# Kernel optimization log

Hardware: AMD Instinct MI355X
Metric: run time of the kernel (lower is better)

The kernel has to match this reference:

```python
import jax, jax.numpy as jnp
import numpy as np
from jax import lax

SOS = -1
BLANK = 28
MAX_SYMBOLS = 4
T, B, ENC = 128, 32, 1024
VOCAB = 29   # includes blank at index 28
EMB = 320
HID = 320


def setup_inputs() -> dict:
    key = jax.random.key(0)
    ks = jax.random.split(key, 9)
    s = 0.1
    return {
        "x": jax.random.normal(ks[0], (T, B, ENC), jnp.float32),
        "lengths": jax.random.randint(ks[1], (B,), T // 2, T + 1, jnp.int32),
        "embedding": jax.random.normal(ks[2], (VOCAB - 1, EMB), jnp.float32) * s,
        "W_ih": jax.random.normal(ks[3], (4 * HID, EMB), jnp.float32) * s,
        "W_hh": jax.random.normal(ks[4], (4 * HID, HID), jnp.float32) * s,
        "b_ih": jax.random.normal(ks[5], (4 * HID,), jnp.float32) * s,
        "b_hh": jax.random.normal(ks[6], (4 * HID,), jnp.float32) * s,
        "W_joint": jax.random.normal(ks[7], (VOCAB, ENC + HID), jnp.float32) * s,
        "b_joint": jax.random.normal(ks[8], (VOCAB,), jnp.float32) * s,
    }


def _lstm_cell(xe, h, c, W_ih, W_hh, b_ih, b_hh):
    gates = xe @ W_ih.T + h @ W_hh.T + b_ih + b_hh          # [B, 4H]
    i, f, g, o = jnp.split(gates, 4, axis=-1)               # torch gate order
    i, f, o = jax.nn.sigmoid(i), jax.nn.sigmoid(f), jax.nn.sigmoid(o)
    g = jnp.tanh(g)
    c2 = f * c + i * g
    h2 = o * jnp.tanh(c2)
    return h2, c2


def _decode(x, lengths, embedding, W_ih, W_hh, b_ih, b_hh, W_joint, b_joint):
    Tn, Bn, _ = x.shape
    Lmax = Tn * MAX_SYMBOLS
    bidx = jnp.arange(Bn)

    def sym_step(carry, _):
        h, c, last, pos, labels, lps, active = carry
        # pred step: zero embedding for SOS, else embed (label>blank -> label-1)
        adj = jnp.where(last > BLANK, last - 1, last)
        adj = jnp.clip(adj, 0, VOCAB - 2)
        emb = jnp.where((last == SOS)[:, None], 0.0, embedding[adj])  # [B, EMB]
        h2, c2 = _lstm_cell(emb, h, c, W_ih, W_hh, b_ih, b_hh)
        # joint step: concat(enc frame, pred) -> fc -> log_softmax
        f_enc = carry_f                                            # closed over
        logits = jnp.concatenate([f_enc, h2], axis=-1) @ W_joint.T + b_joint
        logp = jax.nn.log_softmax(logits, axis=-1)                 # [B, V]
        idx = jnp.argmax(logp, axis=-1).astype(jnp.int32)
        v = jnp.take_along_axis(logp, idx[:, None].astype(jnp.int32), axis=-1)[:, 0]
        is_blank = idx == BLANK
        emit = active & (~is_blank)
        # commit hidden/label only on non-blank emission (as original)
        h = jnp.where(emit[:, None], h2, h)
        c = jnp.where(emit[:, None], c2, c)
        last = jnp.where(emit, idx, last)
        cur = labels[bidx, pos]
        labels = labels.at[bidx, pos].set(jnp.where(emit, idx, cur))
        lps = lps + jnp.where(active, v, 0.0)
        pos = pos + emit.astype(pos.dtype)
        active = active & (~is_blank)
        return (h, c, last, pos, labels, lps, active), None

    def time_step(carry, inp):
        f_t, t = inp                                              # f_t: [B, ENC]
        h, c, last, pos, labels, lps = carry
        active0 = t < lengths
        global carry_f
        carry_f = f_t
        (h, c, last, pos, labels, lps, _), _ = lax.scan(
            sym_step, (h, c, last, pos, labels, lps, active0), None,
            length=MAX_SYMBOLS)
        return (h, c, last, pos, labels, lps), None

    init = (
        jnp.zeros((Bn, HID), x.dtype),
        jnp.zeros((Bn, HID), x.dtype),
        jnp.full((Bn,), SOS, jnp.int32),
        jnp.zeros((Bn,), jnp.int32),
        jnp.full((Bn, Lmax), -1, jnp.int32),
        jnp.zeros((Bn,), x.dtype),
    )
    (h, c, last, pos, labels, lps), _ = lax.scan(
        time_step, init, (x, jnp.arange(Tn)))
    return labels, pos, lps


def reference(x, lengths, embedding, W_ih, W_hh, b_ih, b_hh, W_joint, b_joint):
    # labels: [B, T*MAX_SYMBOLS] int32, padded with -1
    # n_symbols: [B] number of emitted symbols per utterance
    # logp_sum: [B] sum of selected max log-probs over all evaluated decode steps
    labels, n_symbols, logp_sum = _decode(
        x, lengths, embedding, W_ih, W_hh, b_ih, b_hh, W_joint, b_joint)
    return labels, n_symbols, logp_sum
```

## Files before the change

### kernel.cpp

```cpp
#include <hip/hip_runtime.h>
#include <math.h>

typedef unsigned long long u64;
typedef unsigned int u32;

#define BN 32
#define TN 128
#define ENCD 1024
#define HID 320
#define NG 1280
#define VN 29
#define BLANKI 28
#define SLICES 8
#define UPS 40
#define ROWS 160
#define JW 1344
#define XSTRIDE 70
#define NPOLL (SLICES*69)

#define E_OFF   0
#define E_SZ    (TN*BN*VN)
#define P_OFF   (E_OFF + E_SZ)
#define P_SZ    (VN*NG)
#define X_OFF   (P_OFF + P_SZ)
#define X_U64S  (2*BN*SLICES*XSTRIDE)

__device__ __forceinline__ float dot4(float4 a, float4 b) {
    return a.x*b.x + a.y*b.y + a.z*b.z + a.w*b.w;
}

__global__ __launch_bounds__(256) void k_enc(const float* __restrict__ x,
        const float* __restrict__ Wj, const float* __restrict__ bj,
        float* __restrict__ E, u64* __restrict__ xchg)
{
    __shared__ float xl[4][1056];
    const int tid = threadIdx.x;
    const int blk = blockIdx.x;
    const int t = blk >> 3, b0 = (blk & 7) * 4;

    if (tid < 35) xchg[(size_t)blk*35 + tid] = 0ull;

    #pragma unroll
    for (int bb = 0; bb < 4; ++bb) {
        const float4* src = (const float4*)(x + ((size_t)(t*BN + b0 + bb))*ENCD);
        float4 v4 = src[tid];
        ((float4*)&xl[bb][0])[tid + (tid >> 5)] = v4;
    }
    __syncthreads();
    if (tid < 232) {
        const int v = tid >> 3, k8 = tid & 7;
        float a0=0.f, a1=0.f, a2=0.f, a3=0.f;
        const float4* wrow = (const float4*)(Wj + (size_t)v*JW) + k8*32;
        const float4* x0 = ((const float4*)&xl[0][0]) + k8*33;
        const float4* x1 = ((const float4*)&xl[1][0]) + k8*33;
        const float4* x2 = ((const float4*)&xl[2][0]) + k8*33;
        const float4* x3 = ((const float4*)&xl[3][0]) + k8*33;
        #pragma unroll 4
        for (int m = 0; m < 32; ++m) {
            float4 w4 = wrow[m];
            a0 += dot4(w4, x0[m]);
            a1 += dot4(w4, x1[m]);
            a2 += dot4(w4, x2[m]);
            a3 += dot4(w4, x3[m]);
        }
        #pragma unroll
        for (int d = 1; d < 8; d <<= 1) {
            a0 += __shfl_xor(a0, d); a1 += __shfl_xor(a1, d);
            a2 += __shfl_xor(a2, d); a3 += __shfl_xor(a3, d);
        }
        if (k8 == 0) {
            float bjv = bj[v];
            E[((size_t)(t*BN + b0+0))*VN + v] = a0 + bjv;
            E[((size_t)(t*BN + b0+1))*VN + v] = a1 + bjv;
            E[((size_t)(t*BN + b0+2))*VN + v] = a2 + bjv;
            E[((size_t)(t*BN + b0+3))*VN + v] = a3 + bjv;
        }
    }
}

__global__ __launch_bounds__(256) void k_pred(const float* __restrict__ emb,
        const float* __restrict__ Wih, const float* __restrict__ bih,
        const float* __restrict__ bhh, float* __restrict__ P)
{
    __shared__ float el[HID];
    const int tid = threadIdx.x, j = blockIdx.x;
    if (tid < 80) {
        float4 v4 = make_float4(0.f, 0.f, 0.f, 0.f);
        if (j < 28) v4 = ((const float4*)(emb + (size_t)j*HID))[tid];
        ((float4*)el)[tid] = v4;
    }
    __syncthreads();
    #pragma unroll
    for (int q = 0; q < 5; ++q) {
        const int r = q*256 + tid;
        float acc = bih[r] + bhh[r];
        const float4* wrow = (const float4*)(Wih + (size_t)r*HID);
        #pragma unroll 8
        for (int k4 = 0; k4 < 80; ++k4)
            acc += dot4(wrow[k4], ((const float4*)el)[k4]);
        P[(size_t)j*NG + r] = acc;
    }
}

__global__ __launch_bounds__(256, 1) void k_dec(const int* __restrict__ lengths,
        const float* __restrict__ Whh, const float* __restrict__ Wj,
        const float* __restrict__ E, const float* __restrict__ P,
        u64* __restrict__ xchg, float* __restrict__ out)
{
    __shared__ float P_lds[VN*ROWS];
    __shared__ float Wjh[VN*UPS];
    __shared__ float h_com[HID];
    __shared__ float h2st[HID];
    __shared__ float c_com[UPS];
    __shared__ float c2st[UPS];
    __shared__ float gates[ROWS];
    __shared__ float plog_l[SLICES*VN];
    __shared__ float lsum[VN];
    __shared__ float E_l[VN];
    __shared__ float pad_force[14000];

    const int tid = threadIdx.x;
    const int bid = blockIdx.x;
    const int b = bid & 31, slice = bid >> 5;
    const int rg = tid >> 3, kg = tid & 7;
    const int lane = tid & 63;

    int len = lengths[b];
    if (len > TN) len = TN;
    if (len < 0) {
        pad_force[tid] = (float)tid;
        h_com[tid & 255] = pad_force[(tid*7) & 13999];
    }

    float4 wq[50];
    #pragma unroll
    for (int q = 0; q < 5; ++q) {
        const int r = rg*5 + q;
        const int gt = r / 40, u = r - gt*40;
        const float4* wrow = (const float4*)(Whh + ((size_t)(gt*HID + slice*UPS + u))*HID + kg*40);
        #pragma unroll
        for (int jb = 0; jb < 10; ++jb) wq[q*10 + jb] = wrow[jb];
    }
    for (int i = tid; i < VN*ROWS; i += 256) {
        const int jj = i / ROWS, r = i - jj*ROWS;
        const int gt = r / 40, u = r - gt*40;
        P_lds[i] = P[(size_t)jj*NG + gt*HID + slice*UPS + u];
    }
    for (int i = tid; i < VN*UPS; i += 256) {
        const int v = i / UPS, k = i - v*UPS;
        Wjh[i] = Wj[(size_t)v*JW + ENCD + slice*UPS + k];
    }
    for (int i = tid; i < HID; i += 256) h_com[i] = 0.f;
    if (tid < UPS) c_com[tid] = 0.f;
    if (slice == 0) for (int i = tid; i < 512; i += 256) out[b*512 + i] = -1.0f;
    __syncthreads();

    float lps = 0.f;
    int pos = 0, jrow = 28, n = 1;
    bool dirty = true;

    for (int t = 0; t < len; ++t) {
        __syncthreads();
        if (tid < VN) E_l[tid] = E[((size_t)(t*BN + b))*VN + tid];
        __syncthreads();

        for (int s = 0; s < 4; ++s) {
            if (dirty) {
                __syncthreads();
                const int par = n & 1;
                const size_t mybase = ((size_t)(par*BN + b)*SLICES + slice)*XSTRIDE;
                float acc[5] = {0.f, 0.f, 0.f, 0.f, 0.f};
                #pragma unroll
                for (int jb = 0; jb < 10; ++jb) {
                    float4 hv = *(const float4*)(h_com + kg*40 + jb*4);
                    #pragma unroll
                    for (int q = 0; q < 5; ++q) acc[q] += dot4(wq[q*10 + jb], hv);
                }
                #pragma unroll
                for (int q = 0; q < 5; ++q) {
                    acc[q] += __shfl_xor(acc[q], 1);
                    acc[q] += __shfl_xor(acc[q], 2);
                    acc[q] += __shfl_xor(acc[q], 4);
                }
                if (kg == 0) {
                    #pragma unroll
                    for (int q = 0; q < 5; ++q) {
                        const int r = rg*5 + q;
                        gates[r] = acc[q] + P_lds[jrow*ROWS + r];
                    }
                }
                __syncthreads();
                if (tid < UPS) {
                    const float gi = gates[tid],      gf = gates[40+tid];
                    const float gg = gates[80+tid],   go = gates[120+tid];
                    const float ii = 1.f/(1.f+expf(-gi));
                    const float ff = 1.f/(1.f+expf(-gf));
                    const float oo = 1.f/(1.f+expf(-go));
                    const float G  = tanhf(gg);
                    const float c2 = ff*c_com[tid] + ii*G;
                    c2st[tid] = c2;
                    const float h2 = oo * tanhf(c2);
                    h2st[slice*UPS + tid] = h2;
                    const u64 pk = ((u64)(u32)n << 32) | (u64)__float_as_uint(h2);
                    __hip_atomic_store(&xchg[mybase + tid], pk,
                                       __ATOMIC_RELAXED, __HIP_MEMORY_SCOPE_AGENT);
                }
                __syncthreads();
                if (tid < 232) {
                    const int v = tid >> 3, k8 = tid & 7;
                    float pp = 0.f;
                    #pragma unroll
                    for (int m2 = 0; m2 < 5; ++m2)
                        pp += Wjh[v*UPS + k8*5 + m2] * h2st[slice*UPS + k8*5 + m2];
                    pp += __shfl_xor(pp, 1);
                    pp += __shfl_xor(pp, 2);
                    pp += __shfl_xor(pp, 4);
                    if (k8 == 0) {
                        const u64 pk = ((u64)(u32)n << 32) | (u64)__float_as_uint(pp);
                        __hip_atomic_store(&xchg[mybase + UPS + v], pk,
                                           __ATOMIC_RELAXED, __HIP_MEMORY_SCOPE_AGENT);
                    }
                }
                {
                    const size_t pbase = ((size_t)(par*BN + b)*SLICES)*XSTRIDE;
                    for (int i = tid; i < NPOLL; i += 256) {
                        const int j2 = i / 69, w = i - j2*69;
                        const u64* ap = &xchg[pbase + (size_t)j2*XSTRIDE + w];
                        u64 v; int cap = 0;
                        do {
                            v = __hip_atomic_load(ap, __ATOMIC_RELAXED,
                                                  __HIP_MEMORY_SCOPE_AGENT);
                        } while ((u32)(v >> 32) != (u32)n && ++cap < (1 << 22));
                        const float f = __uint_as_float((u32)v);
                        if (w < UPS) h2st[j2*UPS + w] = f;
                        else         plog_l[j2*VN + (w - UPS)] = f;
                    }
                }
                __syncthreads();
                if (tid < VN) {
                    float sA = 0.f;
                    #pragma unroll
                    for (int j2 = 0; j2 < 8; ++j2) sA += plog_l[j2*VN + tid];
                    lsum[tid] = sA;
                }
                __syncthreads();
                n++;
            }
            const float Lv = (lane < VN) ? (E_l[lane] + lsum[lane]) : -INFINITY;
            float m = Lv; int ai = lane;
            #pragma unroll
            for (int d = 1; d < 64; d <<= 1) {
                const float om = __shfl_xor(m, d);
                const int   oi = __shfl_xor(ai, d);
                if (om > m || (om == m && oi < ai)) { m = om; ai = oi; }
            }
            float e = (lane < VN) ? expf(Lv - m) : 0.f;
            #pragma unroll
            for (int d = 1; d < 64; d <<= 1) e += __shfl_xor(e, d);
            lps += -logf(e);

            if (ai == BLANKI) { dirty = false; break; }
            if (slice == 0 && tid == 0) out[b*512 + pos] = (float)ai;
            pos++;
            h_com[tid] = h2st[tid];
            if (tid < 64) h_com[256 + tid] = h2st[256 + tid];
            if (tid < UPS) c_com[tid] = c2st[tid];
            jrow = ai;
            dirty = true;
        }
    }

    if (slice == 0 && tid == 0) {
        out[16384 + b] = (float)pos;
        out[16416 + b] = lps;
    }
}

extern "C" void kernel_launch(void* const* d_in, const int* in_sizes, int n_in,
                              void* d_out, int out_size, void* d_ws, size_t ws_size,
                              hipStream_t stream) {
    const float* x    = (const float*)d_in[0];
    const int* lens   = (const int*)  d_in[1];
    const float* emb  = (const float*)d_in[2];
    const float* Wih  = (const float*)d_in[3];
    const float* Whh  = (const float*)d_in[4];
    const float* bih  = (const float*)d_in[5];
    const float* bhh  = (const float*)d_in[6];
    const float* Wj   = (const float*)d_in[7];
    const float* bj   = (const float*)d_in[8];
    float* out = (float*)d_out;
    float* ws  = (float*)d_ws;

    float* E    = ws + E_OFF;
    float* P    = ws + P_OFF;
    u64*   xchg = (u64*)(ws + X_OFF);

    hipLaunchKernelGGL(k_enc,  dim3(1024), dim3(256), 0, stream, x, Wj, bj, E, xchg);
    hipLaunchKernelGGL(k_pred, dim3(29),   dim3(256), 0, stream, emb, Wih, bih, bhh, P);
    hipLaunchKernelGGL(k_dec,  dim3(256),  dim3(256), 0, stream,
                       lens, Whh, Wj, E, P, xchg, out);
}
```

Before: 2.010 ms.

## Exchange only h2 across slices, compute joint locally, use XCC-local atomic polling

Each slice now broadcasts only its 40 h2 values, not h2 plus partial joint logits. Every block holds the full hidden-part joint weights in LDS and computes the full 29-logit projection locally, which removes one exchange phase and one barrier per decode step. The code probes whether all slices of a batch row share an XCC and, if so, uses inline-asm atomic swap/or operations for the exchange, with a fallback to agent-scope atomics. The encoder logits are kept in registers instead of LDS. In exchange each block does redundant joint compute, and correctness depends on hardware-specific inline asm and an XCC-ID heuristic.

```diff
diff --git a/kernel.cpp b/kernel.cpp
--- a/kernel.cpp
+++ b/kernel.cpp
@@ -15,8 +15,9 @@
 #define UPS 40
 #define ROWS 160
 #define JW 1344
-#define XSTRIDE 70
-#define NPOLL (SLICES*69)
+#define JSTR 324
+#define XSTRIDE 48
+#define NPOLL (7*UPS)
 
 #define E_OFF   0
 #define E_SZ    (TN*BN*VN)
@@ -24,9 +25,37 @@
 #define P_SZ    (VN*NG)
 #define X_OFF   (P_OFF + P_SZ)
 #define X_U64S  (2*BN*SLICES*XSTRIDE)
+#define TOK_OFF X_U64S
+#define DEC_OFF (TOK_OFF + BN*SLICES*16)
+#define HS2_OFF (DEC_OFF + BN)
+#define TOTAL_U64S (HS2_OFF + BN*SLICES)
 
 __device__ __forceinline__ float dot4(float4 a, float4 b) {
     return a.x*b.x + a.y*b.y + a.z*b.z + a.w*b.w;
+}
+
+__device__ __forceinline__ void fast_store(u64* p, u64 v) {
+    asm volatile("global_atomic_swap_x2 %0, %1, off"
+                 :: "v"(p), "v"(v) : "memory");
+}
+__device__ __forceinline__ u64 fast_load(u64* p) {
+    u64 r;
+    asm volatile("global_atomic_or_x2 %0, %1, %2, off sc0\n\ts_waitcnt vmcnt(0)"
+                 : "=&v"(r) : "v"(p), "v"(0ull) : "memory");
+    return r;
+}
+__device__ __forceinline__ void fast_load2(u64* pA, u64* pB, u64& rA, u64& rB) {
+    asm volatile("global_atomic_or_x2 %0, %2, %4, off sc0\n\t"
+                 "global_atomic_or_x2 %1, %3, %4, off sc0\n\t"
+                 "s_waitcnt vmcnt(0)"
+                 : "=&v"(rA), "=&v"(rB)
+                 : "v"(pA), "v"(pB), "v"(0ull) : "memory");
+}
+__device__ __forceinline__ u64 aload(const u64* p) {
+    return __hip_atomic_load(p, __ATOMIC_RELAXED, __HIP_MEMORY_SCOPE_AGENT);
+}
+__device__ __forceinline__ void astore(u64* p, u64 v) {
+    __hip_atomic_store(p, v, __ATOMIC_RELAXED, __HIP_MEMORY_SCOPE_AGENT);
 }
 
 __global__ __launch_bounds__(256) void k_enc(const float* __restrict__ x,
@@ -38,7 +67,10 @@
     const int blk = blockIdx.x;
     const int t = blk >> 3, b0 = (blk & 7) * 4;
 
-    if (tid < 35) xchg[(size_t)blk*35 + tid] = 0ull;
+    if (tid < 29) {
+        const int idx = blk*29 + tid;
+        if (idx < TOTAL_U64S) xchg[idx] = 0ull;
+    }
 
     #pragma unroll
     for (int bb = 0; bb < 4; ++bb) {
@@ -108,16 +140,15 @@
         u64* __restrict__ xchg, float* __restrict__ out)
 {
     __shared__ float P_lds[VN*ROWS];
-    __shared__ float Wjh[VN*UPS];
+    __shared__ float Wjh[VN*JSTR];
     __shared__ float h_com[HID];
     __shared__ float h2st[HID];
     __shared__ float c_com[UPS];
     __shared__ float c2st[UPS];
     __shared__ float gates[ROWS];
-    __shared__ float plog_l[SLICES*VN];
     __shared__ float lsum[VN];
-    __shared__ float E_l[VN];
-    __shared__ float pad_force[14000];
+    __shared__ int   flag_fast;
+    __shared__ float pad_force[6200];
 
     const int tid = threadIdx.x;
     const int bid = blockIdx.x;
@@ -125,11 +156,18 @@
     const int rg = tid >> 3, kg = tid & 7;
     const int lane = tid & 63;
 
+    if (tid == 0) {
+        u32 xcc;
+        asm volatile("s_getreg_b32 %0, hwreg(HW_REG_XCC_ID)" : "=s"(xcc));
+        astore(&xchg[HS2_OFF + b*SLICES + slice], (u64)(xcc & 0xFFu) | 0x100ull);
+        fast_store(&xchg[TOK_OFF + (size_t)(b*SLICES + slice)*16], 0xA5ull);
+    }
+
     int len = lengths[b];
     if (len > TN) len = TN;
     if (len < 0) {
         pad_force[tid] = (float)tid;
-        h_com[tid & 255] = pad_force[(tid*7) & 13999];
+        h_com[tid & 255] = pad_force[(tid*7) & 6199];
     }
 
     float4 wq[50];
@@ -146,23 +184,53 @@
         const int gt = r / 40, u = r - gt*40;
         P_lds[i] = P[(size_t)jj*NG + gt*HID + slice*UPS + u];
     }
-    for (int i = tid; i < VN*UPS; i += 256) {
-        const int v = i / UPS, k = i - v*UPS;
-        Wjh[i] = Wj[(size_t)v*JW + ENCD + slice*UPS + k];
+    for (int i = tid; i < VN*HID; i += 256) {
+        const int v = i / HID, k = i - v*HID;
+        Wjh[v*JSTR + k] = Wj[(size_t)v*JW + ENCD + k];
     }
     for (int i = tid; i < HID; i += 256) h_com[i] = 0.f;
     if (tid < UPS) c_com[tid] = 0.f;
     if (slice == 0) for (int i = tid; i < 512; i += 256) out[b*512 + i] = -1.0f;
+
+    if (tid == 0) {
+        if (slice == 0) {
+            bool ok = true; u32 v0 = 0;
+            for (int j2 = 0; j2 < SLICES; ++j2) {
+                u64 v = 0; int cap = 0;
+                do { v = aload(&xchg[HS2_OFF + b*SLICES + j2]); }
+                while (!(v & 0x100ull) && ++cap < (1 << 22));
+                if (!(v & 0x100ull)) { ok = false; break; }
+                const u32 xv = (u32)(v & 0xFFu);
+                if (xv >= 8u) { ok = false; break; }
+                if (j2 == 0) v0 = xv; else if (xv != v0) { ok = false; break; }
+            }
+            if (ok) {
+                for (int j2 = 1; j2 < SLICES && ok; ++j2) {
+                    u64 v = 0; int cap = 0;
+                    do { v = fast_load(&xchg[TOK_OFF + (size_t)(b*SLICES + j2)*16]); }
+                    while (v != 0xA5ull && ++cap < (1 << 20));
+                    if (v != 0xA5ull) ok = false;
+                }
+            }
+            astore(&xchg[DEC_OFF + b], 2ull | (ok ? 1ull : 0ull));
+            flag_fast = ok ? 1 : 0;
+        } else {
+            u64 v = 0; int cap = 0;
+            do { v = aload(&xchg[DEC_OFF + b]); }
+            while (!(v & 2ull) && ++cap < (1 << 24));
+            flag_fast = (v & 2ull) ? (int)(v & 1ull) : 0;
+        }
+    }
     __syncthreads();
+    const bool fast = (flag_fast != 0);
 
     float lps = 0.f;
     int pos = 0, jrow = 28, n = 1;
     bool dirty = true;
 
     for (int t = 0; t < len; ++t) {
-        __syncthreads();
-        if (tid < VN) E_l[tid] = E[((size_t)(t*BN + b))*VN + tid];
-        __syncthreads();
+        const float Ereg = (lane < VN)
+            ? E[((size_t)(t*BN + b))*VN + lane] : -INFINITY;
 
         for (int s = 0; s < 4; ++s) {
             if (dirty) {
@@ -202,51 +270,67 @@
                     const float h2 = oo * tanhf(c2);
                     h2st[slice*UPS + tid] = h2;
                     const u64 pk = ((u64)(u32)n << 32) | (u64)__float_as_uint(h2);
-                    __hip_atomic_store(&xchg[mybase + tid], pk,
-                                       __ATOMIC_RELAXED, __HIP_MEMORY_SCOPE_AGENT);
+                    u64* p = &xchg[mybase + tid];
+                    if (fast) fast_store(p, pk); else astore(p, pk);
+                }
+                {
+                    const size_t pbase = ((size_t)(par*BN + b)*SLICES)*XSTRIDE;
+                    const int iA = tid;
+                    int jA = iA / UPS; const int wA = iA - jA*UPS;
+                    jA += (jA >= slice);
+                    u64* pA = &xchg[pbase + (size_t)jA*XSTRIDE + wA];
+                    const int iB = tid + 256;
+                    bool needB = (iB < NPOLL);
+                    int jB = 0, wB = 0; u64* pB = pA;
+                    if (needB) {
+                        jB = iB / UPS; wB = iB - jB*UPS; jB += (jB >= slice);
+                        pB = &xchg[pbase + (size_t)jB*XSTRIDE + wB];
+                    }
+                    bool needA = true;
+                    u64 vA = 0, vB = 0;
+                    int cap = 0;
+                    while ((needA || needB) && cap < (1 << 18)) {
+                        if (fast) {
+                            if (needA && needB) fast_load2(pA, pB, vA, vB);
+                            else if (needA)     vA = fast_load(pA);
+                            else                vB = fast_load(pB);
+                        } else {
+                            if (needA) vA = aload(pA);
+                            if (needB) vB = aload(pB);
+                        }
+                        if (needA && (u32)(vA >> 32) == (u32)n) {
+                            h2st[jA*UPS + wA] = __uint_as_float((u32)vA);
+                            needA = false;
+                        }
+                        if (needB && (u32)(vB >> 32) == (u32)n) {
+                            h2st[jB*UPS + wB] = __uint_as_float((u32)vB);
+                            needB = false;
+                        }
+                        ++cap;
+                    }
                 }
                 __syncthreads();
                 if (tid < 232) {
                     const int v = tid >> 3, k8 = tid & 7;
-                    float pp = 0.f;
-                    #pragma unroll
-                    for (int m2 = 0; m2 < 5; ++m2)
-                        pp += Wjh[v*UPS + k8*5 + m2] * h2st[slice*UPS + k8*5 + m2];
-                    pp += __shfl_xor(pp, 1);
-                    pp += __shfl_xor(pp, 2);
-                    pp += __shfl_xor(pp, 4);
-                    if (k8 == 0) {
-                        const u64 pk = ((u64)(u32)n << 32) | (u64)__float_as_uint(pp);
-                        __hip_atomic_store(&xchg[mybase + UPS + v], pk,
-                                           __ATOMIC_RELAXED, __HIP_MEMORY_SCOPE_AGENT);
-                    }
-                }
-                {
-                    const size_t pbase = ((size_t)(par*BN + b)*SLICES)*XSTRIDE;
-                    for (int i = tid; i < NPOLL; i += 256) {
-                        const int j2 = i / 69, w = i - j2*69;
-                        const u64* ap = &xchg[pbase + (size_t)j2*XSTRIDE + w];
-                        u64 v; int cap = 0;
-                        do {
-                            v = __hip_atomic_load(ap, __ATOMIC_RELAXED,
-                                                  __HIP_MEMORY_SCOPE_AGENT);
-                        } while ((u32)(v >> 32) != (u32)n && ++cap < (1 << 22));
-                        const float f = __uint_as_float((u32)v);
-                        if (w < UPS) h2st[j2*UPS + w] = f;
-                        else         plog_l[j2*VN + (w - UPS)] = f;
-                    }
-                }
-                __syncthreads();
-                if (tid < VN) {
                     float sA = 0.f;
                     #pragma unroll
-                    for (int j2 = 0; j2 < 8; ++j2) sA += plog_l[j2*VN + tid];
-                    lsum[tid] = sA;
+                    for (int j2 = 0; j2 < SLICES; ++j2) {
+                        float pp = 0.f;
+                        #pragma unroll
+                        for (int m2 = 0; m2 < 5; ++m2)
+                            pp += Wjh[v*JSTR + j2*UPS + k8*5 + m2]
+                                * h2st[j2*UPS + k8*5 + m2];
+                        pp += __shfl_xor(pp, 1);
+                        pp += __shfl_xor(pp, 2);
+                        pp += __shfl_xor(pp, 4);
+                        sA += pp;
+                    }
+                    if (k8 == 0) lsum[v] = sA;
                 }
                 __syncthreads();
                 n++;
             }
-            const float Lv = (lane < VN) ? (E_l[lane] + lsum[lane]) : -INFINITY;
+            const float Lv = (lane < VN) ? (Ereg + lsum[lane]) : -INFINITY;
             float m = Lv; int ai = lane;
             #pragma unroll
             for (int d = 1; d < 64; d <<= 1) {
```

After: 2.139 ms. 6.4% more time.

## Overlap remote polling with local LSTM/joint compute and drop barriers

Applied to the files above, without the earlier changes.

Splits the block into warp roles: the first wavefront computes the local LSTM cell update and joint partial logits, while the other three wavefronts poll the seven remote slices concurrently, each handling up to three addresses per loop iteration. The own slice is no longer polled. The encoder logit row is held in a register instead of LDS, which removes two barriers per time step. The logit-sum reduction moves into the argmax lane, and the Wjh LDS stride is padded to avoid bank conflicts. The change lowers the spin cap, which risks reading stale values when a wait runs long.

```diff
diff --git a/kernel.cpp b/kernel.cpp
--- a/kernel.cpp
+++ b/kernel.cpp
@@ -15,8 +15,9 @@
 #define UPS 40
 #define ROWS 160
 #define JW 1344
+#define JSTR 41
 #define XSTRIDE 70
-#define NPOLL (SLICES*69)
+#define NPOLL (7*69)
 
 #define E_OFF   0
 #define E_SZ    (TN*BN*VN)
@@ -27,6 +28,12 @@
 
 __device__ __forceinline__ float dot4(float4 a, float4 b) {
     return a.x*b.x + a.y*b.y + a.z*b.z + a.w*b.w;
+}
+__device__ __forceinline__ u64 aload(const u64* p) {
+    return __hip_atomic_load(p, __ATOMIC_RELAXED, __HIP_MEMORY_SCOPE_AGENT);
+}
+__device__ __forceinline__ void astore(u64* p, u64 v) {
+    __hip_atomic_store(p, v, __ATOMIC_RELAXED, __HIP_MEMORY_SCOPE_AGENT);
 }
 
 __global__ __launch_bounds__(256) void k_enc(const float* __restrict__ x,
@@ -108,16 +115,14 @@
         u64* __restrict__ xchg, float* __restrict__ out)
 {
     __shared__ float P_lds[VN*ROWS];
-    __shared__ float Wjh[VN*UPS];
+    __shared__ float Wjh[VN*JSTR];
     __shared__ float h_com[HID];
     __shared__ float h2st[HID];
     __shared__ float c_com[UPS];
     __shared__ float c2st[UPS];
     __shared__ float gates[ROWS];
     __shared__ float plog_l[SLICES*VN];
-    __shared__ float lsum[VN];
-    __shared__ float E_l[VN];
-    __shared__ float pad_force[14000];
+    __shared__ float pad_force[13600];
 
     const int tid = threadIdx.x;
     const int bid = blockIdx.x;
@@ -129,7 +134,7 @@
     if (len > TN) len = TN;
     if (len < 0) {
         pad_force[tid] = (float)tid;
-        h_com[tid & 255] = pad_force[(tid*7) & 13999];
+        h_com[tid & 255] = pad_force[(tid*7) & 13599];
     }
 
     float4 wq[50];
@@ -148,7 +153,7 @@
     }
     for (int i = tid; i < VN*UPS; i += 256) {
         const int v = i / UPS, k = i - v*UPS;
-        Wjh[i] = Wj[(size_t)v*JW + ENCD + slice*UPS + k];
+        Wjh[v*JSTR + k] = Wj[(size_t)v*JW + ENCD + slice*UPS + k];
     }
     for (int i = tid; i < HID; i += 256) h_com[i] = 0.f;
     if (tid < UPS) c_com[tid] = 0.f;
@@ -160,9 +165,8 @@
     bool dirty = true;
 
     for (int t = 0; t < len; ++t) {
-        __syncthreads();
-        if (tid < VN) E_l[tid] = E[((size_t)(t*BN + b))*VN + tid];
-        __syncthreads();
+        const float Ereg = (lane < VN)
+            ? E[((size_t)(t*BN + b))*VN + lane] : -INFINITY;
 
         for (int s = 0; s < 4; ++s) {
             if (dirty) {
@@ -190,63 +194,84 @@
                     }
                 }
                 __syncthreads();
-                if (tid < UPS) {
-                    const float gi = gates[tid],      gf = gates[40+tid];
-                    const float gg = gates[80+tid],   go = gates[120+tid];
-                    const float ii = 1.f/(1.f+expf(-gi));
-                    const float ff = 1.f/(1.f+expf(-gf));
-                    const float oo = 1.f/(1.f+expf(-go));
-                    const float G  = tanhf(gg);
-                    const float c2 = ff*c_com[tid] + ii*G;
-                    c2st[tid] = c2;
-                    const float h2 = oo * tanhf(c2);
-                    h2st[slice*UPS + tid] = h2;
-                    const u64 pk = ((u64)(u32)n << 32) | (u64)__float_as_uint(h2);
-                    __hip_atomic_store(&xchg[mybase + tid], pk,
-                                       __ATOMIC_RELAXED, __HIP_MEMORY_SCOPE_AGENT);
-                }
-                __syncthreads();
-                if (tid < 232) {
-                    const int v = tid >> 3, k8 = tid & 7;
-                    float pp = 0.f;
+                if (tid < 64) {
+                    if (tid < UPS) {
+                        const float gi = gates[tid],      gf = gates[40+tid];
+                        const float gg = gates[80+tid],   go = gates[120+tid];
+                        const float ii = 1.f/(1.f+expf(-gi));
+                        const float ff = 1.f/(1.f+expf(-gf));
+                        const float oo = 1.f/(1.f+expf(-go));
+                        const float G  = tanhf(gg);
+                        const float c2 = ff*c_com[tid] + ii*G;
+                        c2st[tid] = c2;
+                        const float h2 = oo * tanhf(c2);
+                        h2st[slice*UPS + tid] = h2;
+                        const u64 pk = ((u64)(u32)n << 32) | (u64)__float_as_uint(h2);
+                        astore(&xchg[mybase + tid], pk);
+                    }
+                    if (tid < VN) {
+                        float pkv[8];
+                        #pragma unroll
+                        for (int k8 = 0; k8 < 8; ++k8) {
+                            float pk = 0.f;
+                            #pragma unroll
+                            for (int m2 = 0; m2 < 5; ++m2)
+                                pk += Wjh[tid*JSTR + k8*5 + m2]
+                                    * h2st[slice*UPS + k8*5 + m2];
+                            pkv[k8] = pk;
+                        }
+                        const float pp = ((pkv[0]+pkv[1])+(pkv[2]+pkv[3]))
+                                       + ((pkv[4]+pkv[5])+(pkv[6]+pkv[7]));
+                        plog_l[slice*VN + tid] = pp;
+                        const u64 pk2 = ((u64)(u32)n << 32) | (u64)__float_as_uint(pp);
+                        astore(&xchg[mybase + UPS + tid], pk2);
+                    }
+                } else {
+                    const size_t pbase = ((size_t)(par*BN + b)*SLICES)*XSTRIDE;
+                    const int i0 = tid - 64;
+                    u64* ap[3]; int jj[3], ww[3]; bool need[3];
                     #pragma unroll
-                    for (int m2 = 0; m2 < 5; ++m2)
-                        pp += Wjh[v*UPS + k8*5 + m2] * h2st[slice*UPS + k8*5 + m2];
-                    pp += __shfl_xor(pp, 1);
-                    pp += __shfl_xor(pp, 2);
-                    pp += __shfl_xor(pp, 4);
-                    if (k8 == 0) {
-                        const u64 pk = ((u64)(u32)n << 32) | (u64)__float_as_uint(pp);
-                        __hip_atomic_store(&xchg[mybase + UPS + v], pk,
-                                           __ATOMIC_RELAXED, __HIP_MEMORY_SCOPE_AGENT);
-                    }
-                }
-                {
-                    const size_t pbase = ((size_t)(par*BN + b)*SLICES)*XSTRIDE;
-                    for (int i = tid; i < NPOLL; i += 256) {
-                        const int j2 = i / 69, w = i - j2*69;
-                        const u64* ap = &xchg[pbase + (size_t)j2*XSTRIDE + w];
-                        u64 v; int cap = 0;
-                        do {
-                            v = __hip_atomic_load(ap, __ATOMIC_RELAXED,
-                                                  __HIP_MEMORY_SCOPE_AGENT);
-                        } while ((u32)(v >> 32) != (u32)n && ++cap < (1 << 22));
-                        const float f = __uint_as_float((u32)v);
-                        if (w < UPS) h2st[j2*UPS + w] = f;
-                        else         plog_l[j2*VN + (w - UPS)] = f;
-                    }
-                }
-                __syncthreads();
-                if (tid < VN) {
-                    float sA = 0.f;
-                    #pragma unroll
-                    for (int j2 = 0; j2 < 8; ++j2) sA += plog_l[j2*VN + tid];
-                    lsum[tid] = sA;
+                    for (int r = 0; r < 3; ++r) {
+                        const int i = i0 + 192*r;
+                        need[r] = (i < NPOLL);
+                        int j2 = 0, w = 0;
+                        if (need[r]) {
+                            j2 = i / 69; w = i - j2*69;
+                            j2 += (j2 >= slice);
+                        }
+                        jj[r] = j2; ww[r] = w;
+                        ap[r] = (u64*)&xchg[pbase + (size_t)j2*XSTRIDE + w];
+                    }
+                    int cap = 0;
+                    while ((need[0] | need[1] | need[2]) && cap < (1 << 16)) {
+                        u64 v[3];
+                        #pragma unroll
+                        for (int r = 0; r < 3; ++r)
+                            if (need[r]) v[r] = aload(ap[r]);
+                        #pragma unroll
+                        for (int r = 0; r < 3; ++r) {
+                            if (need[r] && (u32)(v[r] >> 32) == (u32)n) {
+                                const float f = __uint_as_float((u32)v[r]);
+                                if (ww[r] < UPS) h2st[jj[r]*UPS + ww[r]] = f;
+                                else             plog_l[jj[r]*VN + (ww[r]-UPS)] = f;
+                                need[r] = false;
+                            }
+                        }
+                        ++cap;
+                    }
                 }
                 __syncthreads();
                 n++;
             }
-            const float Lv = (lane < VN) ? (E_l[lane] + lsum[lane]) : -INFINITY;
+            float Lv;
+            if (lane < VN) {
+                float sA = 0.f;
+                #pragma unroll
+                for (int j2 = 0; j2 < SLICES; ++j2) sA += plog_l[j2*VN + lane];
+                Lv = Ereg + sA;
+            } else {
+                Lv = -INFINITY;
+            }
             float m = Lv; int ai = lane;
             #pragma unroll
             for (int d = 1; d < 64; d <<= 1) {
```

New measurement: 1.785 ms. 1.13x faster.
